# Optimization experiments

Measured on AMD Instinct MI355X. Metric: run time of the kernel, lower is better.

Reference implementation:

```python
import jax, jax.numpy as jnp
import numpy as np
import math

B, S, D = 8, 4096, 128  # batch, seq_len, embed_dim == attention_head_size
EPS = 1e-5


def layer_norm(x, w, b):
    mu = jnp.mean(x, axis=-1, keepdims=True)
    var = jnp.var(x, axis=-1, keepdims=True)
    return (x - mu) * jax.lax.rsqrt(var + EPS) * w + b


def setup_inputs() -> dict:
    key = jax.random.key(0)
    ks = jax.random.split(key, 4)
    x = jax.random.normal(ks[0], (B, S, D), dtype=jnp.float32)
    Wq = jax.random.normal(ks[1], (D, D), dtype=jnp.float32) / math.sqrt(D)
    Wk = jax.random.normal(ks[2], (D, D), dtype=jnp.float32) / math.sqrt(D)
    Wv = jax.random.normal(ks[3], (D, D), dtype=jnp.float32) / math.sqrt(D)
    qn_w = jnp.ones((D,), dtype=jnp.float32)
    qn_b = jnp.zeros((D,), dtype=jnp.float32)
    kn_w = jnp.ones((D,), dtype=jnp.float32)
    kn_b = jnp.zeros((D,), dtype=jnp.float32)
    return {"x": x, "Wq": Wq, "Wk": Wk, "Wv": Wv,
            "qn_w": qn_w, "qn_b": qn_b, "kn_w": kn_w, "kn_b": kn_b}


def reference(x, Wq, Wk, Wv, qn_w, qn_b, kn_w, kn_b):
    # q/k/v projections (nn.Linear with no bias: x @ W^T)
    q = layer_norm(jnp.einsum('bsd,hd->bsh', x, Wq), qn_w, qn_b)
    k = layer_norm(jnp.einsum('bsd,hd->bsh', x, Wk), kn_w, kn_b)
    v = jnp.einsum('bsd,hd->bsh', x, Wv)
    scale = math.sqrt(D)
    scores = jnp.einsum('bqh,bkh->bqk', q, k) / scale  # [B, S, S]
    attn = jax.nn.softmax(scores, axis=-1)
    # dropout_rate = 0.0 -> identity
    return jnp.einsum('bqk,bkh->bqh', attn, v)
```

## Files before the change

kernel.cpp:

```cpp
#include <hip/hip_runtime.h>

#define B_ 8
#define S_ 4096
#define D_ 128
#define KVB 64
#define NT (S_ / KVB)

typedef __attribute__((ext_vector_type(4))) float f32x4;
typedef __attribute__((ext_vector_type(8))) short s16x8;

__device__ __forceinline__ unsigned short f2bf(float f) {
    union { float f; unsigned u; } v; v.f = f;
    unsigned r = (v.u + 0x7fffu + ((v.u >> 16) & 1u)) >> 16;
    return (unsigned short)r;
}

__device__ __forceinline__ unsigned cvt_pk(float lo, float hi) {
    unsigned r;
    asm("v_cvt_pk_bf16_f32 %0, %1, %2" : "=v"(r) : "v"(lo), "v"(hi));
    return r;
}

__device__ __forceinline__ s16x8 load_cvt8(const float* p) {
    f32x4 a = *(const f32x4*)p;
    f32x4 b = *(const f32x4*)(p + 4);
    s16x8 r;
    r[0] = (short)f2bf(a[0]); r[1] = (short)f2bf(a[1]);
    r[2] = (short)f2bf(a[2]); r[3] = (short)f2bf(a[3]);
    r[4] = (short)f2bf(b[0]); r[5] = (short)f2bf(b[1]);
    r[6] = (short)f2bf(b[2]); r[7] = (short)f2bf(b[3]);
    return r;
}

__device__ __forceinline__ void gld16(unsigned short* lds, const unsigned short* g) {
    __builtin_amdgcn_global_load_lds(
        (const __attribute__((address_space(1))) unsigned int*)g,
        (__attribute__((address_space(3))) unsigned int*)lds,
        16, 0, 0);
}

__global__ __launch_bounds__(256, 1) void proj_kernel(
    const float* __restrict__ x,  const float* __restrict__ Wq,
    const float* __restrict__ Wk, const float* __restrict__ Wv,
    const float* __restrict__ qn_w, const float* __restrict__ qn_b,
    const float* __restrict__ kn_w, const float* __restrict__ kn_b,
    unsigned short* __restrict__ qo, unsigned short* __restrict__ ko,
    unsigned short* __restrict__ vto)
{
    __shared__ unsigned short wlds[128 * 136];
    __shared__ unsigned short vstage[128 * 72];

    const int tid  = threadIdx.x;
    const int lane = tid & 63;
    const int wv   = tid >> 6;
    const int j    = lane & 15;
    const int g    = lane >> 4;

    const int b    = blockIdx.x >> 6;
    const int sblk = (blockIdx.x & 63) * 64;
    const int srow = sblk + wv * 16;

    const float* xrow = x + ((size_t)b * S_ + srow + j) * D_;
    s16x8 af[4];
#pragma unroll
    for (int kk = 0; kk < 4; ++kk) af[kk] = load_cvt8(xrow + kk * 32 + g * 8);

    const int wrow = tid >> 1;
    const int wcol = (tid & 1) * 64;

#pragma unroll 1
    for (int m = 0; m < 3; ++m) {
        const float* Wm = (m == 0) ? Wq : (m == 1) ? Wk : Wv;
        __syncthreads();
#pragma unroll
        for (int it = 0; it < 8; ++it) {
            int col = wcol + it * 8;
            *(s16x8*)&wlds[wrow * 136 + col] = load_cvt8(Wm + wrow * 128 + col);
        }
        __syncthreads();

        f32x4 acc[8];
#pragma unroll
        for (int ct = 0; ct < 8; ++ct) { f32x4 z = {0.f, 0.f, 0.f, 0.f}; acc[ct] = z; }
#pragma unroll
        for (int ct = 0; ct < 8; ++ct) {
#pragma unroll
            for (int kk = 0; kk < 4; ++kk) {
                s16x8 bf = *(const s16x8*)&wlds[(ct * 16 + j) * 136 + kk * 32 + g * 8];
                acc[ct] = __builtin_amdgcn_mfma_f32_16x16x32_bf16(af[kk], bf, acc[ct], 0, 0, 0);
            }
        }

        if (m < 2) {
            const float* lw = (m == 0) ? qn_w : kn_w;
            const float* lb = (m == 0) ? qn_b : kn_b;
            float sum[4], sq[4];
#pragma unroll
            for (int r = 0; r < 4; ++r) {
                float s1 = 0.f, s2 = 0.f;
#pragma unroll
                for (int ct = 0; ct < 8; ++ct) { float v = acc[ct][r]; s1 += v; s2 += v * v; }
#pragma unroll
                for (int msk = 1; msk < 16; msk <<= 1) {
                    s1 += __shfl_xor(s1, msk);
                    s2 += __shfl_xor(s2, msk);
                }
                sum[r] = s1; sq[r] = s2;
            }
            float gwv[8], gbv[8];
#pragma unroll
            for (int ct = 0; ct < 8; ++ct) { gwv[ct] = lw[ct * 16 + j]; gbv[ct] = lb[ct * 16 + j]; }
            unsigned short* dst = (m == 0) ? qo : ko;
            const float post = (m == 0) ? 0.12751742361888f : 1.0f;
#pragma unroll
            for (int r = 0; r < 4; ++r) {
                float mean = sum[r] * (1.f / 128.f);
                float var  = sq[r] * (1.f / 128.f) - mean * mean;
                float rstd = rsqrtf(var + 1e-5f);
                size_t rowoff = ((size_t)b * S_ + sblk + wv * 16 + g * 4 + r) * D_;
#pragma unroll
                for (int ct = 0; ct < 8; ++ct) {
                    float val = ((acc[ct][r] - mean) * rstd * gwv[ct] + gbv[ct]) * post;
                    dst[rowoff + ct * 16 + j] = f2bf(val);
                }
            }
        } else {
#pragma unroll
            for (int ct = 0; ct < 8; ++ct) {
#pragma unroll
                for (int r = 0; r < 4; ++r) {
                    vstage[(ct * 16 + j) * 72 + wv * 16 + g * 4 + r] = f2bf(acc[ct][r]);
                }
            }
            __syncthreads();
            int h  = tid >> 1;
            int cb = (tid & 1) * 32;
#pragma unroll
            for (int c = 0; c < 4; ++c) {
                *(s16x8*)(vto + ((size_t)b * D_ + h) * S_ + sblk + cb + c * 8) =
                    *(const s16x8*)&vstage[h * 72 + cb + c * 8];
            }
        }
    }
}

__global__ __launch_bounds__(256, 2) void attn_kernel(
    const unsigned short* __restrict__ qb, const unsigned short* __restrict__ kb,
    const unsigned short* __restrict__ vtb, float* __restrict__ out)
{
    __shared__ unsigned short kbuf[2][KVB * D_];
    __shared__ unsigned short vbuf[2][D_ * KVB];

    const int tid  = threadIdx.x;
    const int lane = tid & 63;
    const int wv   = tid >> 6;
    const int qg   = wv & 1;
    const int kh   = wv >> 1;
    const int j    = lane & 15;
    const int g    = lane >> 4;

    const int swz = (blockIdx.x & 7) * 64 + (blockIdx.x >> 3);
    const int b   = swz >> 6;
    const int s0  = (swz & 63) * 64;

    const unsigned short* qr0 = qb + ((size_t)b * S_ + s0 + qg * 32 + j) * D_;
    const unsigned short* qr1 = qr0 + 16 * D_;
    s16x8 qf0[4], qf1[4];
#pragma unroll
    for (int kk = 0; kk < 4; ++kk) {
        qf0[kk] = *(const s16x8*)(qr0 + kk * 32 + g * 8);
        qf1[kk] = *(const s16x8*)(qr1 + kk * 32 + g * 8);
    }

    const unsigned short* kg_base = kb  + (size_t)b * S_ * D_;
    const unsigned short* vg_base = vtb + (size_t)b * D_ * S_;

    auto STAGE = [&](int bi, int kt) {
        const int kv0 = kt * KVB;
#pragma unroll
        for (int it = 0; it < 4; ++it) {
            const int row = wv * 16 + it * 4 + (lane >> 4);
            const int fk  = (row & 3) | (((row >> 3) & 1) << 2);
            const unsigned short* src =
                kg_base + (size_t)(kv0 + row) * D_ + (((lane & 15) ^ fk) << 3);
            gld16(&kbuf[bi][(wv * 16 + it * 4) * D_], src);
        }
#pragma unroll
        for (int it = 0; it < 4; ++it) {
            const int h = wv * 32 + it * 8 + (lane >> 3);
            const unsigned short* src =
                vg_base + (size_t)h * S_ + kv0 + (((lane & 7) ^ (h & 7)) << 3);
            gld16(&vbuf[bi][(wv * 32 + it * 8) * KVB], src);
        }
    };

    STAGE(0, 0);
    STAGE(1, 1);

    f32x4 acc[2][8];
#pragma unroll
    for (int qs = 0; qs < 2; ++qs)
#pragma unroll
        for (int ht = 0; ht < 8; ++ht) { f32x4 z = {0.f,0.f,0.f,0.f}; acc[qs][ht] = z; }
    f32x4 acc_l[2];
    { f32x4 z = {0.f,0.f,0.f,0.f}; acc_l[0] = z; acc_l[1] = z; }

    s16x8 ones;
#pragma unroll
    for (int e = 0; e < 8; ++e) ones[e] = (short)0x3F80;

    const int fKj   = j & 7;
    const int prow0 = 8 * (j >> 2) + (j & 3) + 32 * kh;
    const int prow1 = prow0 + 4;

    s16x8 vfr[8];
    union PU { unsigned u[4]; s16x8 v; };
    PU P0, P1;

    auto PV_PREV = [&]() {
        __builtin_amdgcn_s_setprio(1);
        acc_l[0] = __builtin_amdgcn_mfma_f32_16x16x32_bf16(P0.v, ones, acc_l[0], 0, 0, 0);
        acc_l[1] = __builtin_amdgcn_mfma_f32_16x16x32_bf16(P1.v, ones, acc_l[1], 0, 0, 0);
#pragma unroll
        for (int ht = 0; ht < 8; ++ht) {
            acc[0][ht] = __builtin_amdgcn_mfma_f32_16x16x32_bf16(P0.v, vfr[ht], acc[0][ht], 0, 0, 0);
            acc[1][ht] = __builtin_amdgcn_mfma_f32_16x16x32_bf16(P1.v, vfr[ht], acc[1][ht], 0, 0, 0);
        }
        __builtin_amdgcn_s_setprio(0);
    };

#pragma unroll 1
    for (int kt = 0; kt < NT; ++kt) {
        const int cur = kt & 1;
        if (kt + 1 < NT) { asm volatile("s_waitcnt vmcnt(8)" ::: "memory"); }
        else             { asm volatile("s_waitcnt vmcnt(0)" ::: "memory"); }
        __builtin_amdgcn_s_barrier();
        asm volatile("" ::: "memory");

        const unsigned short* kl = kbuf[cur];
        const unsigned short* vl = vbuf[cur];

        s16x8 kf[8];
#pragma unroll
        for (int kk = 0; kk < 4; ++kk) {
            const int cs = (((kk * 4 + g) ^ fKj) << 3);
            kf[kk * 2 + 0] = *(const s16x8*)&kl[prow0 * D_ + cs];
            kf[kk * 2 + 1] = *(const s16x8*)&kl[prow1 * D_ + cs];
        }

        if (kt) PV_PREV();

        f32x4 sv[2][2];
#pragma unroll
        for (int qs = 0; qs < 2; ++qs) {
            f32x4 z = {0.f,0.f,0.f,0.f}; sv[qs][0] = z; sv[qs][1] = z;
        }
        __builtin_amdgcn_s_setprio(1);
#pragma unroll
        for (int kk = 0; kk < 4; ++kk) {
            sv[0][0] = __builtin_amdgcn_mfma_f32_16x16x32_bf16(kf[kk*2+0], qf0[kk], sv[0][0], 0, 0, 0);
            sv[1][0] = __builtin_amdgcn_mfma_f32_16x16x32_bf16(kf[kk*2+0], qf1[kk], sv[1][0], 0, 0, 0);
            sv[0][1] = __builtin_amdgcn_mfma_f32_16x16x32_bf16(kf[kk*2+1], qf0[kk], sv[0][1], 0, 0, 0);
            sv[1][1] = __builtin_amdgcn_mfma_f32_16x16x32_bf16(kf[kk*2+1], qf1[kk], sv[1][1], 0, 0, 0);
        }
        __builtin_amdgcn_s_setprio(0);

#pragma unroll
        for (int ht = 0; ht < 8; ++ht) {
            vfr[ht] = *(const s16x8*)&vl[(ht * 16 + j) * KVB + (((4 * kh + g) ^ fKj) << 3)];
        }

        float p0[8], p1[8];
#pragma unroll
        for (int r = 0; r < 4; ++r) {
            p0[r]     = exp2f(sv[0][0][r]);
            p0[4 + r] = exp2f(sv[0][1][r]);
            p1[r]     = exp2f(sv[1][0][r]);
            p1[4 + r] = exp2f(sv[1][1][r]);
        }
        P0.u[0] = cvt_pk(p0[0], p0[1]); P0.u[1] = cvt_pk(p0[2], p0[3]);
        P0.u[2] = cvt_pk(p0[4], p0[5]); P0.u[3] = cvt_pk(p0[6], p0[7]);
        P1.u[0] = cvt_pk(p1[0], p1[1]); P1.u[1] = cvt_pk(p1[2], p1[3]);
        P1.u[2] = cvt_pk(p1[4], p1[5]); P1.u[3] = cvt_pk(p1[6], p1[7]);

        asm volatile("s_waitcnt lgkmcnt(0)" ::: "memory");
        __builtin_amdgcn_s_barrier();
        asm volatile("" ::: "memory");
        if (kt + 2 < NT) STAGE(cur, kt + 2);
    }

    PV_PREV();

    float* csum = (float*)&kbuf[0][0];
    float* lsum = (float*)&vbuf[0][0];
    if (kh == 1) {
#pragma unroll
        for (int qs = 0; qs < 2; ++qs) {
#pragma unroll
            for (int ht = 0; ht < 8; ++ht)
                *(f32x4*)&csum[(((qg * 2 + qs) * 8 + ht) * 64 + lane) * 4] = acc[qs][ht];
            *(f32x4*)&lsum[((qg * 2 + qs) * 64 + lane) * 4] = acc_l[qs];
        }
    }
    __syncthreads();
    if (kh == 0) {
#pragma unroll
        for (int qs = 0; qs < 2; ++qs) {
            f32x4 lt = *(const f32x4*)&lsum[((qg * 2 + qs) * 64 + lane) * 4];
            f32x4 li;
#pragma unroll
            for (int r = 0; r < 4; ++r) li[r] = 1.0f / (acc_l[qs][r] + lt[r]);
#pragma unroll
            for (int ht = 0; ht < 8; ++ht) {
                f32x4 o = *(const f32x4*)&csum[(((qg * 2 + qs) * 8 + ht) * 64 + lane) * 4];
                size_t base = ((size_t)b * S_ + s0 + qg * 32 + qs * 16 + g * 4) * D_ + ht * 16 + j;
                out[base         ] = (acc[qs][ht][0] + o[0]) * li[0];
                out[base +     D_] = (acc[qs][ht][1] + o[1]) * li[1];
                out[base + 2 * D_] = (acc[qs][ht][2] + o[2]) * li[2];
                out[base + 3 * D_] = (acc[qs][ht][3] + o[3]) * li[3];
            }
        }
    }
}

extern "C" void kernel_launch(void* const* d_in, const int* in_sizes, int n_in,
                              void* d_out, int out_size, void* d_ws, size_t ws_size,
                              hipStream_t stream) {
    const float* x    = (const float*)d_in[0];
    const float* Wq   = (const float*)d_in[1];
    const float* Wk   = (const float*)d_in[2];
    const float* Wv   = (const float*)d_in[3];
    const float* qn_w = (const float*)d_in[4];
    const float* qn_b = (const float*)d_in[5];
    const float* kn_w = (const float*)d_in[6];
    const float* kn_b = (const float*)d_in[7];
    float* out = (float*)d_out;

    const size_t n = (size_t)B_ * S_ * D_;
    unsigned short* qws  = (unsigned short*)d_ws;
    unsigned short* kws  = qws + n;
    unsigned short* vtws = kws + n;

    proj_kernel<<<512, 256, 0, stream>>>(x, Wq, Wk, Wv, qn_w, qn_b, kn_w, kn_b,
                                         qws, kws, vtws);
    attn_kernel<<<512, 256, 0, stream>>>(qws, kws, vtws, out);
}
```

Before: 120.0 us.

## Load V fragments directly from global and triple-buffer K to drop a barrier

Stops staging V tiles through shared memory: each lane now reads its transposed-V fragments straight from global memory into registers, one KV tile ahead of the P·V MFMAs. K tiles move to a three-slot LDS ring, so the end-of-iteration waitcnt and barrier that protected buffer reuse are removed and the vmcnt wait is simplified. This cuts LDS traffic, shared memory size and one barrier per iteration. The cost is strided, less coalesced global reads of V that rely on L2 hits, plus more register-held outstanding loads.

```diff
diff --git a/kernel.cpp b/kernel.cpp
--- a/kernel.cpp
+++ b/kernel.cpp
@@ -148,8 +148,7 @@
     const unsigned short* __restrict__ qb, const unsigned short* __restrict__ kb,
     const unsigned short* __restrict__ vtb, float* __restrict__ out)
 {
-    __shared__ unsigned short kbuf[2][KVB * D_];
-    __shared__ unsigned short vbuf[2][D_ * KVB];
+    __shared__ unsigned short kbuf[3][KVB * D_];
 
     const int tid  = threadIdx.x;
     const int lane = tid & 63;
@@ -172,10 +171,11 @@
         qf1[kk] = *(const s16x8*)(qr1 + kk * 32 + g * 8);
     }
 
-    const unsigned short* kg_base = kb  + (size_t)b * S_ * D_;
-    const unsigned short* vg_base = vtb + (size_t)b * D_ * S_;
-
-    auto STAGE = [&](int bi, int kt) {
+    const unsigned short* kg_base = kb + (size_t)b * S_ * D_;
+    const unsigned short* vlane =
+        vtb + (size_t)b * D_ * S_ + (size_t)j * S_ + 32 * kh + 8 * g;
+
+    auto STAGE_K = [&](int bi, int kt) {
         const int kv0 = kt * KVB;
 #pragma unroll
         for (int it = 0; it < 4; ++it) {
@@ -185,17 +185,10 @@
                 kg_base + (size_t)(kv0 + row) * D_ + (((lane & 15) ^ fk) << 3);
             gld16(&kbuf[bi][(wv * 16 + it * 4) * D_], src);
         }
-#pragma unroll
-        for (int it = 0; it < 4; ++it) {
-            const int h = wv * 32 + it * 8 + (lane >> 3);
-            const unsigned short* src =
-                vg_base + (size_t)h * S_ + kv0 + (((lane & 7) ^ (h & 7)) << 3);
-            gld16(&vbuf[bi][(wv * 32 + it * 8) * KVB], src);
-        }
     };
 
-    STAGE(0, 0);
-    STAGE(1, 1);
+    STAGE_K(0, 0);
+    STAGE_K(1, 1);
 
     f32x4 acc[2][8];
 #pragma unroll
@@ -229,16 +222,14 @@
         __builtin_amdgcn_s_setprio(0);
     };
 
+    int cur = 0;
 #pragma unroll 1
     for (int kt = 0; kt < NT; ++kt) {
-        const int cur = kt & 1;
-        if (kt + 1 < NT) { asm volatile("s_waitcnt vmcnt(8)" ::: "memory"); }
-        else             { asm volatile("s_waitcnt vmcnt(0)" ::: "memory"); }
+        asm volatile("s_waitcnt vmcnt(4)" ::: "memory");
         __builtin_amdgcn_s_barrier();
         asm volatile("" ::: "memory");
 
         const unsigned short* kl = kbuf[cur];
-        const unsigned short* vl = vbuf[cur];
 
         s16x8 kf[8];
 #pragma unroll
@@ -249,6 +240,13 @@
         }
 
         if (kt) PV_PREV();
+
+        {
+            const unsigned short* vt_t = vlane + kt * KVB;
+#pragma unroll
+            for (int ht = 0; ht < 8; ++ht)
+                vfr[ht] = *(const s16x8*)(vt_t + (size_t)ht * 16 * S_);
+        }
 
         f32x4 sv[2][2];
 #pragma unroll
@@ -265,11 +263,6 @@
         }
         __builtin_amdgcn_s_setprio(0);
 
-#pragma unroll
-        for (int ht = 0; ht < 8; ++ht) {
-            vfr[ht] = *(const s16x8*)&vl[(ht * 16 + j) * KVB + (((4 * kh + g) ^ fKj) << 3)];
-        }
-
         float p0[8], p1[8];
 #pragma unroll
         for (int r = 0; r < 4; ++r) {
@@ -283,16 +276,19 @@
         P1.u[0] = cvt_pk(p1[0], p1[1]); P1.u[1] = cvt_pk(p1[2], p1[3]);
         P1.u[2] = cvt_pk(p1[4], p1[5]); P1.u[3] = cvt_pk(p1[6], p1[7]);
 
-        asm volatile("s_waitcnt lgkmcnt(0)" ::: "memory");
-        __builtin_amdgcn_s_barrier();
-        asm volatile("" ::: "memory");
-        if (kt + 2 < NT) STAGE(cur, kt + 2);
+        if (kt + 2 < NT) {
+            int nxt = cur + 2; if (nxt >= 3) nxt -= 3;
+            STAGE_K(nxt, kt + 2);
+        }
+        ++cur; if (cur == 3) cur = 0;
     }
 
     PV_PREV();
 
+    __syncthreads();
+
     float* csum = (float*)&kbuf[0][0];
-    float* lsum = (float*)&vbuf[0][0];
+    float* lsum = (float*)&kbuf[2][0];
     if (kh == 1) {
 #pragma unroll
         for (int qs = 0; qs < 2; ++qs) {
```

After: 166.5 us. +38.8%, slower.

## Switch attention MFMAs from 16x16x32 to 32x32x16 tiles

Applied to the files above, without the earlier changes.

Replaces the 16x16x32 bf16 MFMA tiling of the QK^T and PV products with 32x32x16 instructions. The K and V LDS swizzles, fragment loads, row permutation and output epilogue are reworked to match the new accumulator layout. Each wave now issues fewer, larger MFMAs, which is meant to cut instruction-issue overhead and raise matrix-core throughput. In exchange the lane-to-row mapping gets more complex, the permutation trick carries correctness risk, and a barrier is added before the final reduction.

```diff
diff --git a/kernel.cpp b/kernel.cpp
--- a/kernel.cpp
+++ b/kernel.cpp
@@ -7,6 +7,7 @@
 #define NT (S_ / KVB)
 
 typedef __attribute__((ext_vector_type(4))) float f32x4;
+typedef __attribute__((ext_vector_type(16))) float f32x16;
 typedef __attribute__((ext_vector_type(8))) short s16x8;
 
 __device__ __forceinline__ unsigned short f2bf(float f) {
@@ -156,40 +157,38 @@
     const int wv   = tid >> 6;
     const int qg   = wv & 1;
     const int kh   = wv >> 1;
-    const int j    = lane & 15;
-    const int g    = lane >> 4;
+    const int a    = lane & 31;
+    const int hh   = lane >> 5;
+
+    const int blk = (a >> 2) & 3;
+    const int pa  = (blk == 1) ? a + 4 : (blk == 2) ? a - 4 : a;
 
     const int swz = (blockIdx.x & 7) * 64 + (blockIdx.x >> 3);
     const int b   = swz >> 6;
     const int s0  = (swz & 63) * 64;
 
-    const unsigned short* qr0 = qb + ((size_t)b * S_ + s0 + qg * 32 + j) * D_;
-    const unsigned short* qr1 = qr0 + 16 * D_;
-    s16x8 qf0[4], qf1[4];
-#pragma unroll
-    for (int kk = 0; kk < 4; ++kk) {
-        qf0[kk] = *(const s16x8*)(qr0 + kk * 32 + g * 8);
-        qf1[kk] = *(const s16x8*)(qr1 + kk * 32 + g * 8);
-    }
+    const unsigned short* qptr = qb + ((size_t)b * S_ + s0 + qg * 32 + a) * D_;
+    s16x8 qf[8];
+#pragma unroll
+    for (int kk = 0; kk < 8; ++kk) qf[kk] = *(const s16x8*)(qptr + kk * 16 + hh * 8);
 
     const unsigned short* kg_base = kb  + (size_t)b * S_ * D_;
     const unsigned short* vg_base = vtb + (size_t)b * D_ * S_;
 
-    auto STAGE = [&](int bi, int kt) {
-        const int kv0 = kt * KVB;
+    auto STAGE = [&](int bi, int kt2) {
+        const int kv0 = kt2 * KVB;
 #pragma unroll
         for (int it = 0; it < 4; ++it) {
             const int row = wv * 16 + it * 4 + (lane >> 4);
-            const int fk  = (row & 3) | (((row >> 3) & 1) << 2);
             const unsigned short* src =
-                kg_base + (size_t)(kv0 + row) * D_ + (((lane & 15) ^ fk) << 3);
+                kg_base + (size_t)(kv0 + row) * D_ + (((lane & 15) ^ (row & 15)) << 3);
             gld16(&kbuf[bi][(wv * 16 + it * 4) * D_], src);
         }
 #pragma unroll
         for (int it = 0; it < 4; ++it) {
-            const int h = wv * 32 + it * 8 + (lane >> 3);
+            const int row = wv * 32 + it * 8 + (lane >> 3);
             const unsigned short* src =
-                vg_base + (size_t)h * S_ + kv0 + (((lane & 7) ^ (h & 7)) << 3);
+                vg_base + (size_t)row * S_ + kv0 + (((lane & 7) ^ ((lane >> 3) & 7)) << 3);
             gld16(&vbuf[bi][(wv * 32 + it * 8) * KVB], src);
         }
     };
@@ -197,21 +196,21 @@
     STAGE(0, 0);
     STAGE(1, 1);
 
-    f32x4 acc[2][8];
-#pragma unroll
-    for (int qs = 0; qs < 2; ++qs)
-#pragma unroll
-        for (int ht = 0; ht < 8; ++ht) { f32x4 z = {0.f,0.f,0.f,0.f}; acc[qs][ht] = z; }
-    f32x4 acc_l[2];
-    { f32x4 z = {0.f,0.f,0.f,0.f}; acc_l[0] = z; acc_l[1] = z; }
+    f32x16 acc[4], ld;
+#pragma unroll
+    for (int dt = 0; dt < 4; ++dt)
+#pragma unroll
+        for (int e = 0; e < 16; ++e) acc[dt][e] = 0.f;
+#pragma unroll
+    for (int e = 0; e < 16; ++e) ld[e] = 0.f;
 
     s16x8 ones;
 #pragma unroll
     for (int e = 0; e < 8; ++e) ones[e] = (short)0x3F80;
 
-    const int fKj   = j & 7;
-    const int prow0 = 8 * (j >> 2) + (j & 3) + 32 * kh;
-    const int prow1 = prow0 + 4;
+    const int kbase = (32 * kh + pa) * D_;
+    const int kswz  = pa & 15;
+    const int vswz  = lane & 7;
 
     s16x8 vfr[8];
     union PU { unsigned u[4]; s16x8 v; };
@@ -219,12 +218,12 @@
 
     auto PV_PREV = [&]() {
         __builtin_amdgcn_s_setprio(1);
-        acc_l[0] = __builtin_amdgcn_mfma_f32_16x16x32_bf16(P0.v, ones, acc_l[0], 0, 0, 0);
-        acc_l[1] = __builtin_amdgcn_mfma_f32_16x16x32_bf16(P1.v, ones, acc_l[1], 0, 0, 0);
-#pragma unroll
-        for (int ht = 0; ht < 8; ++ht) {
-            acc[0][ht] = __builtin_amdgcn_mfma_f32_16x16x32_bf16(P0.v, vfr[ht], acc[0][ht], 0, 0, 0);
-            acc[1][ht] = __builtin_amdgcn_mfma_f32_16x16x32_bf16(P1.v, vfr[ht], acc[1][ht], 0, 0, 0);
+        ld = __builtin_amdgcn_mfma_f32_32x32x16_bf16(P0.v, ones, ld, 0, 0, 0);
+        ld = __builtin_amdgcn_mfma_f32_32x32x16_bf16(P1.v, ones, ld, 0, 0, 0);
+#pragma unroll
+        for (int dt = 0; dt < 4; ++dt) {
+            acc[dt] = __builtin_amdgcn_mfma_f32_32x32x16_bf16(P0.v, vfr[dt * 2 + 0], acc[dt], 0, 0, 0);
+            acc[dt] = __builtin_amdgcn_mfma_f32_32x32x16_bf16(P1.v, vfr[dt * 2 + 1], acc[dt], 0, 0, 0);
         }
         __builtin_amdgcn_s_setprio(0);
     };
@@ -242,46 +241,34 @@
 
         s16x8 kf[8];
 #pragma unroll
-        for (int kk = 0; kk < 4; ++kk) {
-            const int cs = (((kk * 4 + g) ^ fKj) << 3);
-            kf[kk * 2 + 0] = *(const s16x8*)&kl[prow0 * D_ + cs];
-            kf[kk * 2 + 1] = *(const s16x8*)&kl[prow1 * D_ + cs];
-        }
+        for (int kk = 0; kk < 8; ++kk)
+            kf[kk] = *(const s16x8*)&kl[kbase + (((2 * kk + hh) ^ kswz) << 3)];
 
         if (kt) PV_PREV();
 
-        f32x4 sv[2][2];
-#pragma unroll
-        for (int qs = 0; qs < 2; ++qs) {
-            f32x4 z = {0.f,0.f,0.f,0.f}; sv[qs][0] = z; sv[qs][1] = z;
-        }
+        f32x16 sv;
+#pragma unroll
+        for (int e = 0; e < 16; ++e) sv[e] = 0.f;
         __builtin_amdgcn_s_setprio(1);
 #pragma unroll
-        for (int kk = 0; kk < 4; ++kk) {
-            sv[0][0] = __builtin_amdgcn_mfma_f32_16x16x32_bf16(kf[kk*2+0], qf0[kk], sv[0][0], 0, 0, 0);
-            sv[1][0] = __builtin_amdgcn_mfma_f32_16x16x32_bf16(kf[kk*2+0], qf1[kk], sv[1][0], 0, 0, 0);
-            sv[0][1] = __builtin_amdgcn_mfma_f32_16x16x32_bf16(kf[kk*2+1], qf0[kk], sv[0][1], 0, 0, 0);
-            sv[1][1] = __builtin_amdgcn_mfma_f32_16x16x32_bf16(kf[kk*2+1], qf1[kk], sv[1][1], 0, 0, 0);
-        }
+        for (int kk = 0; kk < 8; ++kk)
+            sv = __builtin_amdgcn_mfma_f32_32x32x16_bf16(kf[kk], qf[kk], sv, 0, 0, 0);
         __builtin_amdgcn_s_setprio(0);
 
 #pragma unroll
-        for (int ht = 0; ht < 8; ++ht) {
-            vfr[ht] = *(const s16x8*)&vl[(ht * 16 + j) * KVB + (((4 * kh + g) ^ fKj) << 3)];
-        }
-
-        float p0[8], p1[8];
-#pragma unroll
-        for (int r = 0; r < 4; ++r) {
-            p0[r]     = exp2f(sv[0][0][r]);
-            p0[4 + r] = exp2f(sv[0][1][r]);
-            p1[r]     = exp2f(sv[1][0][r]);
-            p1[4 + r] = exp2f(sv[1][1][r]);
-        }
-        P0.u[0] = cvt_pk(p0[0], p0[1]); P0.u[1] = cvt_pk(p0[2], p0[3]);
-        P0.u[2] = cvt_pk(p0[4], p0[5]); P0.u[3] = cvt_pk(p0[6], p0[7]);
-        P1.u[0] = cvt_pk(p1[0], p1[1]); P1.u[1] = cvt_pk(p1[2], p1[3]);
-        P1.u[2] = cvt_pk(p1[4], p1[5]); P1.u[3] = cvt_pk(p1[6], p1[7]);
+        for (int dt = 0; dt < 4; ++dt)
+#pragma unroll
+            for (int km = 0; km < 2; ++km)
+                vfr[dt * 2 + km] = *(const s16x8*)
+                    &vl[(32 * dt + a) * KVB + (((4 * kh + 2 * km + hh) ^ vswz) << 3)];
+
+        float p[16];
+#pragma unroll
+        for (int e = 0; e < 16; ++e) p[e] = exp2f(sv[e]);
+        P0.u[0] = cvt_pk(p[0],  p[1]);  P0.u[1] = cvt_pk(p[2],  p[3]);
+        P0.u[2] = cvt_pk(p[4],  p[5]);  P0.u[3] = cvt_pk(p[6],  p[7]);
+        P1.u[0] = cvt_pk(p[8],  p[9]);  P1.u[1] = cvt_pk(p[10], p[11]);
+        P1.u[2] = cvt_pk(p[12], p[13]); P1.u[3] = cvt_pk(p[14], p[15]);
 
         asm volatile("s_waitcnt lgkmcnt(0)" ::: "memory");
         __builtin_amdgcn_s_barrier();
@@ -291,33 +278,45 @@
 
     PV_PREV();
 
+    __syncthreads();
+
     float* csum = (float*)&kbuf[0][0];
     float* lsum = (float*)&vbuf[0][0];
     if (kh == 1) {
 #pragma unroll
-        for (int qs = 0; qs < 2; ++qs) {
-#pragma unroll
-            for (int ht = 0; ht < 8; ++ht)
-                *(f32x4*)&csum[(((qg * 2 + qs) * 8 + ht) * 64 + lane) * 4] = acc[qs][ht];
-            *(f32x4*)&lsum[((qg * 2 + qs) * 64 + lane) * 4] = acc_l[qs];
+        for (int dt = 0; dt < 4; ++dt)
+#pragma unroll
+            for (int rr = 0; rr < 4; ++rr) {
+                f32x4 c4 = { acc[dt][rr*4+0], acc[dt][rr*4+1], acc[dt][rr*4+2], acc[dt][rr*4+3] };
+                *(f32x4*)&csum[((qg * 4 + dt) * 4 + rr) * 256 + lane * 4] = c4;
+            }
+#pragma unroll
+        for (int rr = 0; rr < 4; ++rr) {
+            f32x4 l4 = { ld[rr*4+0], ld[rr*4+1], ld[rr*4+2], ld[rr*4+3] };
+            *(f32x4*)&lsum[(qg * 4 + rr) * 256 + lane * 4] = l4;
         }
     }
     __syncthreads();
     if (kh == 0) {
-#pragma unroll
-        for (int qs = 0; qs < 2; ++qs) {
-            f32x4 lt = *(const f32x4*)&lsum[((qg * 2 + qs) * 64 + lane) * 4];
-            f32x4 li;
-#pragma unroll
-            for (int r = 0; r < 4; ++r) li[r] = 1.0f / (acc_l[qs][r] + lt[r]);
-#pragma unroll
-            for (int ht = 0; ht < 8; ++ht) {
-                f32x4 o = *(const f32x4*)&csum[(((qg * 2 + qs) * 8 + ht) * 64 + lane) * 4];
-                size_t base = ((size_t)b * S_ + s0 + qg * 32 + qs * 16 + g * 4) * D_ + ht * 16 + j;
-                out[base         ] = (acc[qs][ht][0] + o[0]) * li[0];
-                out[base +     D_] = (acc[qs][ht][1] + o[1]) * li[1];
-                out[base + 2 * D_] = (acc[qs][ht][2] + o[2]) * li[2];
-                out[base + 3 * D_] = (acc[qs][ht][3] + o[3]) * li[3];
+        float li[16];
+#pragma unroll
+        for (int rr = 0; rr < 4; ++rr) {
+            f32x4 lt = *(const f32x4*)&lsum[(qg * 4 + rr) * 256 + lane * 4];
+#pragma unroll
+            for (int e = 0; e < 4; ++e) li[rr * 4 + e] = 1.0f / (ld[rr * 4 + e] + lt[e]);
+        }
+#pragma unroll
+        for (int dt = 0; dt < 4; ++dt) {
+#pragma unroll
+            for (int rr = 0; rr < 4; ++rr) {
+                f32x4 o4 = *(const f32x4*)&csum[((qg * 4 + dt) * 4 + rr) * 256 + lane * 4];
+#pragma unroll
+                for (int e = 0; e < 4; ++e) {
+                    const int r = rr * 4 + e;
+                    const int qrow = (r & 3) + 8 * (r >> 2) + 4 * hh;
+                    out[((size_t)b * S_ + s0 + qg * 32 + qrow) * D_ + 32 * dt + a] =
+                        (acc[dt][r] + o4[e]) * li[r];
+                }
             }
         }
     }
```

Result: slower. 129.3 us (+7.8%).

## Re-swizzle K/V shared tiles, split V by key half, stagger KV start

Applied to the files above, without the earlier changes.

Changes the K tile XOR swizzle to use the full row index, and splits the V tile into two per-key-half sub-buffers with 32-element rows and a new swizzle, so each kh wave group reads its own contiguous sub-tile. This is meant to cut LDS bank conflicts. It also rotates the starting KV tile for alternate blocks (koff) so neighbouring blocks read different K/V regions at the same time, spreading L2/HBM traffic. A __syncthreads is added before the epilogue reuses the shared buffers.

```diff
diff --git a/kernel.cpp b/kernel.cpp
--- a/kernel.cpp
+++ b/kernel.cpp
@@ -149,7 +149,7 @@
     const unsigned short* __restrict__ vtb, float* __restrict__ out)
 {
     __shared__ unsigned short kbuf[2][KVB * D_];
-    __shared__ unsigned short vbuf[2][D_ * KVB];
+    __shared__ unsigned short vbuf[2][2][D_ * 32];
 
     const int tid  = threadIdx.x;
     const int lane = tid & 63;
@@ -163,6 +163,8 @@
     const int b   = swz >> 6;
     const int s0  = (swz & 63) * 64;
 
+    const int koff = ((blockIdx.x >> 3) & 1) * (NT / 2);
+
     const unsigned short* qr0 = qb + ((size_t)b * S_ + s0 + qg * 32 + j) * D_;
     const unsigned short* qr1 = qr0 + 16 * D_;
     s16x8 qf0[4], qf1[4];
@@ -175,27 +177,29 @@
     const unsigned short* kg_base = kb  + (size_t)b * S_ * D_;
     const unsigned short* vg_base = vtb + (size_t)b * D_ * S_;
 
-    auto STAGE = [&](int bi, int kt) {
-        const int kv0 = kt * KVB;
+    auto STAGE = [&](int bi, int kt2) {
+        const int kv0 = kt2 * KVB;
 #pragma unroll
         for (int it = 0; it < 4; ++it) {
             const int row = wv * 16 + it * 4 + (lane >> 4);
-            const int fk  = (row & 3) | (((row >> 3) & 1) << 2);
             const unsigned short* src =
-                kg_base + (size_t)(kv0 + row) * D_ + (((lane & 15) ^ fk) << 3);
+                kg_base + (size_t)(kv0 + row) * D_ + (((lane & 15) ^ (row & 15)) << 3);
             gld16(&kbuf[bi][(wv * 16 + it * 4) * D_], src);
         }
+        const int ksub = wv & 1;
+        const int rb   = 64 * (wv >> 1);
 #pragma unroll
         for (int it = 0; it < 4; ++it) {
-            const int h = wv * 32 + it * 8 + (lane >> 3);
+            const int row = rb + it * 16 + (lane >> 2);
+            const int gg  = (row ^ (row >> 2)) & 3;
             const unsigned short* src =
-                vg_base + (size_t)h * S_ + kv0 + (((lane & 7) ^ (h & 7)) << 3);
-            gld16(&vbuf[bi][(wv * 32 + it * 8) * KVB], src);
+                vg_base + (size_t)row * S_ + kv0 + ksub * 32 + (((lane & 3) ^ gg) << 3);
+            gld16(&vbuf[bi][ksub][(rb + it * 16) * 32], src);
         }
     };
 
-    STAGE(0, 0);
-    STAGE(1, 1);
+    STAGE(0, koff);
+    STAGE(1, (1 + koff) & (NT - 1));
 
     f32x4 acc[2][8];
 #pragma unroll
@@ -209,9 +213,10 @@
 #pragma unroll
     for (int e = 0; e < 8; ++e) ones[e] = (short)0x3F80;
 
-    const int fKj   = j & 7;
     const int prow0 = 8 * (j >> 2) + (j & 3) + 32 * kh;
     const int prow1 = prow0 + 4;
+    const int ksz0  = prow0 & 15;
+    const int ksz1  = prow1 & 15;
 
     s16x8 vfr[8];
     union PU { unsigned u[4]; s16x8 v; };
@@ -238,14 +243,13 @@
         asm volatile("" ::: "memory");
 
         const unsigned short* kl = kbuf[cur];
-        const unsigned short* vl = vbuf[cur];
+        const unsigned short* vl = vbuf[cur][kh];
 
         s16x8 kf[8];
 #pragma unroll
         for (int kk = 0; kk < 4; ++kk) {
-            const int cs = (((kk * 4 + g) ^ fKj) << 3);
-            kf[kk * 2 + 0] = *(const s16x8*)&kl[prow0 * D_ + cs];
-            kf[kk * 2 + 1] = *(const s16x8*)&kl[prow1 * D_ + cs];
+            kf[kk * 2 + 0] = *(const s16x8*)&kl[prow0 * D_ + (((kk * 4 + g) ^ ksz0) << 3)];
+            kf[kk * 2 + 1] = *(const s16x8*)&kl[prow1 * D_ + (((kk * 4 + g) ^ ksz1) << 3)];
         }
 
         if (kt) PV_PREV();
@@ -267,7 +271,9 @@
 
 #pragma unroll
         for (int ht = 0; ht < 8; ++ht) {
-            vfr[ht] = *(const s16x8*)&vl[(ht * 16 + j) * KVB + (((4 * kh + g) ^ fKj) << 3)];
+            const int row = ht * 16 + j;
+            const int gg  = (row ^ (row >> 2)) & 3;
+            vfr[ht] = *(const s16x8*)&vl[row * 32 + ((g ^ gg) << 3)];
         }
 
         float p0[8], p1[8];
@@ -286,13 +292,15 @@
         asm volatile("s_waitcnt lgkmcnt(0)" ::: "memory");
         __builtin_amdgcn_s_barrier();
         asm volatile("" ::: "memory");
-        if (kt + 2 < NT) STAGE(cur, kt + 2);
+        if (kt + 2 < NT) STAGE(cur, (kt + 2 + koff) & (NT - 1));
     }
 
     PV_PREV();
 
+    __syncthreads();
+
     float* csum = (float*)&kbuf[0][0];
-    float* lsum = (float*)&vbuf[0][0];
+    float* lsum = (float*)&vbuf[0][0][0];
     if (kh == 1) {
 #pragma unroll
         for (int qs = 0; qs < 2; ++qs) {
```

Result: no change. 118.2 us (-1.5%).
